# Kernel optimization log

Measured on AMD Instinct MI355X. Metric: run time of the kernel, lower is better.

The kernel has to match this reference:

```python
import jax, jax.numpy as jnp
import numpy as np

N_EXPERTS = 64
LN_EPS = 1e-5


def _layer_norm(x, gamma, beta, eps=LN_EPS):
    mu = jnp.mean(x, axis=-1, keepdims=True)
    var = jnp.mean(jnp.square(x - mu), axis=-1, keepdims=True)
    return (x - mu) * jax.lax.rsqrt(var + eps) * gamma + beta


def setup_inputs() -> dict:
    key = jax.random.key(0)
    ks = jax.random.split(key, 4)
    B, T, D, Ff = 2, 1024, 512, 2048
    x = jax.random.normal(ks[0], (B, T, D), dtype=jnp.float32)
    hex_weights = jax.random.uniform(ks[1], (B, T, N_EXPERTS), dtype=jnp.float32)
    W_in = jax.random.normal(ks[2], (N_EXPERTS, Ff, D), dtype=jnp.float32) * (D ** -0.5)
    b_in = jnp.zeros((N_EXPERTS, Ff), dtype=jnp.float32)
    W_out = jax.random.normal(ks[3], (N_EXPERTS, D, Ff), dtype=jnp.float32) * (Ff ** -0.5)
    b_out = jnp.zeros((N_EXPERTS, D), dtype=jnp.float32)
    ln_gamma = jnp.ones((D,), dtype=jnp.float32)
    ln_beta = jnp.zeros((D,), dtype=jnp.float32)
    return {"x": x, "hex_weights": hex_weights, "W_in": W_in, "b_in": b_in,
            "W_out": W_out, "b_out": b_out, "ln_gamma": ln_gamma,
            "ln_beta": ln_beta, "top_k": 4}


def reference(x, hex_weights, W_in, b_in, W_out, b_out, ln_gamma, ln_beta, top_k):
    B, T, D = x.shape
    N = B * T
    x_n = _layer_norm(x, ln_gamma, ln_beta)

    # top-k routing; renormalize the selected weights (matches torch topk + sum-norm)
    top_w, top_idx = jax.lax.top_k(hex_weights, top_k)          # (B,T,k)
    top_w = top_w / (jnp.sum(top_w, axis=-1, keepdims=True) + 1e-8)

    x_flat = x_n.reshape(N, D)
    # Scatter the k normalized weights into a dense (N, 64) routing matrix.
    # Non-selected experts get weight 0, so a dense per-expert sweep computes
    # EXACTLY the same combined output as the per-token gather in the original.
    w_full = jnp.zeros((N, N_EXPERTS), dtype=x.dtype)
    w_full = w_full.at[jnp.arange(N)[:, None], top_idx.reshape(N, top_k)].set(
        top_w.reshape(N, top_k))

    def body(acc, e):
        W_in_e, b_in_e, W_out_e, b_out_e, we = e  # we: (N,)
        h = jax.nn.silu(x_flat @ W_in_e.T + b_in_e)            # (N, d_ff)
        acc = acc + we[:, None] * (h @ W_out_e.T + b_out_e)    # (N, D)
        return acc, None

    acc, _ = jax.lax.scan(body, jnp.zeros_like(x_flat),
                          (W_in, b_in, W_out, b_out, w_full.T))
    return acc.reshape(B, T, D)
```

## Files before the change

kernel.cpp:

```cpp
#include <hip/hip_runtime.h>

#define NTOK 2048
#define DD   512
#define FFD  2048
#define NE   64
#define KSEL 4
#define NPAIR (NTOK*KSEL)
#define BM 192
#define BK 64
#define NT 128
#define HROWS (NPAIR + 256)

typedef short s16x8 __attribute__((ext_vector_type(8)));
typedef float f32x4 __attribute__((ext_vector_type(4)));

typedef const __attribute__((address_space(1))) char* gptr_t;
typedef __attribute__((address_space(3))) char* lptr_t;

static __device__ __forceinline__ unsigned short f2bf(float f) {
    unsigned int u = __builtin_bit_cast(unsigned int, f);
    u += 0x7FFFu + ((u >> 16) & 1u);
    return (unsigned short)(u >> 16);
}

static __device__ __forceinline__ void packwrite(char* base, int nn, int kb, float4 v) {
    unsigned int lo = (unsigned int)f2bf(v.x) | ((unsigned int)f2bf(v.y) << 16);
    unsigned int hi = (unsigned int)f2bf(v.z) | ((unsigned int)f2bf(v.w) << 16);
    *(uint2*)(base + nn * 128 + (kb ^ ((nn & 7) << 4))) = make_uint2(lo, hi);
}

__global__ __launch_bounds__(256) void k_ln_route(
    const float* __restrict__ x, const float* __restrict__ hw,
    const float* __restrict__ gamma, const float* __restrict__ beta,
    unsigned short* __restrict__ xn_bf, int* __restrict__ counts,
    int* __restrict__ tok_e, float* __restrict__ tok_w)
{
    const int t = blockIdx.x;
    const int tid = threadIdx.x;
    const float* xr = x + (size_t)t * DD;
    float v0 = xr[tid];
    float v1 = xr[tid + 256];
    float s = v0 + v1, s2 = v0*v0 + v1*v1;
    #pragma unroll
    for (int off = 32; off > 0; off >>= 1) {
        s  += __shfl_down(s, off);
        s2 += __shfl_down(s2, off);
    }
    __shared__ float rsum[4], rsum2[4];
    __shared__ float smu, srs;
    const int wid = tid >> 6, lane = tid & 63;
    if (lane == 0) { rsum[wid] = s; rsum2[wid] = s2; }
    __syncthreads();
    if (tid == 0) {
        float a = 0.f, b = 0.f;
        for (int i = 0; i < 4; ++i) { a += rsum[i]; b += rsum2[i]; }
        float mu  = a * (1.f / DD);
        float var = b * (1.f / DD) - mu * mu;
        smu = mu; srs = rsqrtf(var + 1e-5f);
    }
    __syncthreads();
    const float mu = smu, rstd = srs;
    xn_bf[(size_t)t*DD + tid]       = f2bf((v0 - mu) * rstd * gamma[tid]       + beta[tid]);
    xn_bf[(size_t)t*DD + tid + 256] = f2bf((v1 - mu) * rstd * gamma[tid + 256] + beta[tid + 256]);

    if (tid < 64) {
        float v = hw[(size_t)t*NE + tid];
        int   sel[KSEL]; float sw[KSEL];
        #pragma unroll
        for (int j = 0; j < KSEL; ++j) {
            float m = v; int mi = tid;
            #pragma unroll
            for (int off = 32; off > 0; off >>= 1) {
                float ov = __shfl_xor(m, off);
                int   oi = __shfl_xor(mi, off);
                if (ov > m || (ov == m && oi < mi)) { m = ov; mi = oi; }
            }
            if (tid == mi) v = -1e30f;
            sel[j] = mi; sw[j] = m;
        }
        if (tid == 0) {
            float ssum = sw[0] + sw[1] + sw[2] + sw[3];
            float inv = 1.f / (ssum + 1e-8f);
            #pragma unroll
            for (int j = 0; j < KSEL; ++j) {
                tok_e[t*KSEL + j] = sel[j];
                tok_w[t*KSEL + j] = sw[j] * inv;
                atomicAdd(&counts[sel[j]], 1);
            }
        }
    }
}

__global__ void k_scan(const int* __restrict__ counts, int* __restrict__ offs,
                       int* __restrict__ cursor, int* __restrict__ tile_e,
                       int* __restrict__ tile_r, int* __restrict__ ntiles)
{
    __shared__ int sc[NE], stc[NE];
    const int tid = threadIdx.x;
    sc[tid] = counts[tid];
    __syncthreads();
    int off = 0;
    for (int i = 0; i < tid; ++i) off += sc[i];
    offs[tid] = off; cursor[tid] = off;
    if (tid == NE-1) offs[NE] = off + sc[NE-1];
    int tc = (sc[tid] + BM - 1) / BM;
    stc[tid] = tc;
    __syncthreads();
    int toff = 0;
    for (int i = 0; i < tid; ++i) toff += stc[i];
    for (int j = 0; j < tc; ++j) { tile_e[toff + j] = tid; tile_r[toff + j] = off + j*BM; }
    if (tid == NE-1) *ntiles = toff + tc;
}

__global__ __launch_bounds__(256) void k_scatter(
    const int* __restrict__ tok_e, const float* __restrict__ tok_w,
    int* __restrict__ cursor, int* __restrict__ pair_tok,
    float* __restrict__ pair_w, int* __restrict__ inv)
{
    int i = blockIdx.x * 256 + threadIdx.x;
    if (i >= NPAIR) return;
    int t = i >> 2;
    int e = tok_e[i];
    int slot = atomicAdd(&cursor[e], 1);
    pair_tok[slot] = t;
    pair_w[slot] = tok_w[i];
    inv[i] = slot;
}

template<int KD, bool IS_IN, int NYG>
__global__ __launch_bounds__(256, 2) void k_moe_gemm(
    const unsigned short* __restrict__ Abf,
    const float* __restrict__ W, const float* __restrict__ bias,
    const int* __restrict__ tile_e, const int* __restrict__ tile_r,
    const int* __restrict__ ntiles, const int* __restrict__ offs,
    const int* __restrict__ pr_tok, const float* __restrict__ pr_w,
    unsigned short* __restrict__ Hout, float* __restrict__ Pout)
{
    constexpr int NK = KD / BK;
    const int ti = ((blockIdx.x >> 3) / NYG) * 8 + (blockIdx.x & 7);
    const int yg = (blockIdx.x >> 3) % NYG;
    if (ti >= *ntiles) return;
    const int e    = tile_e[ti];
    const int row0 = tile_r[ti];
    const int rend = offs[e + 1];
    const int n0   = yg * 64;
    const int NOUT = IS_IN ? FFD : DD;

    __shared__ __align__(16) unsigned short As[2 * BM * BK];
    __shared__ __align__(16) unsigned short Bs[2 * 64 * BK];

    const int tid  = threadIdx.x;
    const int lane = tid & 63, wave = tid >> 6;
    const int wmbase = wave * 48;

    const char* asrc[6];
    #pragma unroll
    for (int i = 0; i < 6; ++i) {
        int seg  = wave * 6 + i;
        int r    = seg * 8 + (lane >> 3);
        int grow = row0 + r;
        int cg   = (lane & 7) ^ (r & 7);
        size_t rowbase;
        if (IS_IN) {
            int tok = (grow < rend) ? pr_tok[grow] : pr_tok[row0];
            rowbase = (size_t)tok * (KD * 2);
        } else {
            rowbase = (size_t)grow * (KD * 2);
        }
        asrc[i] = (const char*)Abf + rowbase + (size_t)cg * 16;
    }

    const float* wsrc0 = W + (size_t)e * NOUT * KD + (size_t)(n0 + (tid >> 4)) * KD + (tid & 15) * 4;
    const int nb = tid >> 4;
    const int kb = (tid & 15) * 8;

    f32x4 acc[3][4];
    #pragma unroll
    for (int m = 0; m < 3; ++m)
        #pragma unroll
        for (int n = 0; n < 4; ++n)
            acc[m][n] = (f32x4){0.f, 0.f, 0.f, 0.f};

    float4 bset0[4], bset1[4];

    #pragma unroll
    for (int i = 0; i < 6; ++i)
        __builtin_amdgcn_global_load_lds((gptr_t)asrc[i],
            (lptr_t)((char*)As + (wave * 6 + i) * 1024), 16, 0, 0);
    __builtin_amdgcn_sched_barrier(0);
    #pragma unroll
    for (int i = 0; i < 4; ++i)
        bset0[i] = *(const float4*)(wsrc0 + (size_t)i * 16 * KD);
    __builtin_amdgcn_sched_barrier(0);
    #pragma unroll
    for (int i = 0; i < 4; ++i)
        bset1[i] = *(const float4*)(wsrc0 + (size_t)i * 16 * KD + BK);
    __builtin_amdgcn_sched_barrier(0);
    asm volatile("s_waitcnt vmcnt(4)" ::: "memory");
    __builtin_amdgcn_sched_barrier(0);
    #pragma unroll
    for (int i = 0; i < 4; ++i)
        packwrite((char*)Bs, nb + i * 16, kb, bset0[i]);

    int buf = 0;

#define GEMM_STEP(KT, SUSE, SISS)                                                        \
    {                                                                                    \
        if ((KT) == NK - 1) {                                                            \
            asm volatile("s_waitcnt vmcnt(0) lgkmcnt(0)" ::: "memory");                  \
        } else {                                                                         \
            asm volatile("s_waitcnt vmcnt(4) lgkmcnt(0)" ::: "memory");                  \
        }                                                                                \
        __builtin_amdgcn_s_barrier();                                                    \
        __builtin_amdgcn_sched_barrier(0);                                               \
        const int nbuf_ = buf ^ 1;                                                       \
        if ((KT) + 1 < NK) {                                                             \
            _Pragma("unroll")                                                            \
            for (int i = 0; i < 6; ++i)                                                  \
                __builtin_amdgcn_global_load_lds(                                        \
                    (gptr_t)(asrc[i] + (size_t)((KT) + 1) * BK * 2),                     \
                    (lptr_t)((char*)As + nbuf_ * (BM * BK * 2) + (wave * 6 + i) * 1024), \
                    16, 0, 0);                                                           \
        }                                                                                \
        __builtin_amdgcn_sched_barrier(0);                                               \
        if ((KT) + 2 < NK) {                                                             \
            _Pragma("unroll")                                                            \
            for (int i = 0; i < 4; ++i)                                                  \
                SISS[i] = *(const float4*)(wsrc0 + (size_t)i * 16 * KD + ((KT) + 2) * BK); \
        }                                                                                \
        __builtin_amdgcn_sched_barrier(0);                                               \
        {                                                                                \
            const char* Ab = (const char*)As + buf * (BM * BK * 2);                      \
            const char* Bb = (const char*)Bs + buf * (64 * BK * 2);                      \
            _Pragma("unroll")                                                            \
            for (int h = 0; h < 2; ++h) {                                                \
                s16x8 af[3], bfr[4];                                                     \
                const int koff = h * 64 + (lane >> 4) * 16;                              \
                _Pragma("unroll")                                                        \
                for (int m = 0; m < 3; ++m) {                                            \
                    int row = wmbase + m * 16 + (lane & 15);                             \
                    af[m] = *(const s16x8*)(Ab + row * 128 + (koff ^ ((row & 7) << 4))); \
                }                                                                        \
                _Pragma("unroll")                                                        \
                for (int n = 0; n < 4; ++n) {                                            \
                    int row = n * 16 + (lane & 15);                                      \
                    bfr[n] = *(const s16x8*)(Bb + row * 128 + (koff ^ ((row & 7) << 4)));\
                }                                                                        \
                _Pragma("unroll")                                                        \
                for (int m = 0; m < 3; ++m)                                              \
                    _Pragma("unroll")                                                    \
                    for (int n = 0; n < 4; ++n)                                          \
                        acc[m][n] = __builtin_amdgcn_mfma_f32_16x16x32_bf16(             \
                            af[m], bfr[n], acc[m][n], 0, 0, 0);                          \
            }                                                                            \
        }                                                                                \
        __builtin_amdgcn_sched_barrier(0);                                               \
        if ((KT) + 1 < NK) {                                                             \
            if ((KT) + 2 < NK) asm volatile("s_waitcnt vmcnt(10)" ::: "memory");         \
            else               asm volatile("s_waitcnt vmcnt(6)" ::: "memory");          \
            __builtin_amdgcn_sched_barrier(0);                                           \
            char* Bw = (char*)Bs + nbuf_ * (64 * BK * 2);                                \
            _Pragma("unroll")                                                            \
            for (int i = 0; i < 4; ++i)                                                  \
                packwrite(Bw, nb + i * 16, kb, SUSE[i]);                                 \
        }                                                                                \
        buf ^= 1;                                                                        \
    }

    for (int kt = 0; kt < NK; kt += 2) {
        GEMM_STEP(kt,     bset1, bset0);
        GEMM_STEP(kt + 1, bset0, bset1);
    }
#undef GEMM_STEP

    #pragma unroll
    for (int m = 0; m < 3; ++m) {
        #pragma unroll
        for (int r = 0; r < 4; ++r) {
            int row = row0 + wmbase + m * 16 + (lane >> 4) * 4 + r;
            if (row < rend) {
                if (IS_IN) {
                    #pragma unroll
                    for (int n = 0; n < 4; ++n) {
                        int f = n0 + n * 16 + (lane & 15);
                        float v = acc[m][n][r] + bias[e * FFD + f];
                        v = v / (1.f + __expf(-v));
                        Hout[(size_t)row * FFD + f] = f2bf(v);
                    }
                } else {
                    float pw = pr_w[row];
                    #pragma unroll
                    for (int n = 0; n < 4; ++n) {
                        int d = n0 + n * 16 + (lane & 15);
                        Pout[(size_t)row * DD + d] = (acc[m][n][r] + bias[e * DD + d]) * pw;
                    }
                }
            }
        }
    }
}

__global__ __launch_bounds__(128) void k_combine(
    const float* __restrict__ pout, const int* __restrict__ inv,
    float* __restrict__ out)
{
    const int t = blockIdx.x;
    const int tid = threadIdx.x;
    const float4* p0 = (const float4*)(pout + (size_t)inv[t*4+0]*DD);
    const float4* p1 = (const float4*)(pout + (size_t)inv[t*4+1]*DD);
    const float4* p2 = (const float4*)(pout + (size_t)inv[t*4+2]*DD);
    const float4* p3 = (const float4*)(pout + (size_t)inv[t*4+3]*DD);
    float4 a = p0[tid], b = p1[tid], c = p2[tid], d = p3[tid];
    float4 r;
    r.x = a.x + b.x + c.x + d.x;
    r.y = a.y + b.y + c.y + d.y;
    r.z = a.z + b.z + c.z + d.z;
    r.w = a.w + b.w + c.w + d.w;
    ((float4*)(out + (size_t)t*DD))[tid] = r;
}

extern "C" void kernel_launch(void* const* d_in, const int* in_sizes, int n_in,
                              void* d_out, int out_size, void* d_ws, size_t ws_size,
                              hipStream_t stream)
{
    const float* x     = (const float*)d_in[0];
    const float* hw    = (const float*)d_in[1];
    const float* Win   = (const float*)d_in[2];
    const float* bin   = (const float*)d_in[3];
    const float* Wout  = (const float*)d_in[4];
    const float* bout  = (const float*)d_in[5];
    const float* gamma = (const float*)d_in[6];
    const float* beta  = (const float*)d_in[7];
    float* out = (float*)d_out;

    char* ws = (char*)d_ws;
    size_t o = 0;
    unsigned short* xn_bf = (unsigned short*)(ws + o); o += (size_t)NTOK * DD * 2;
    unsigned short* H     = (unsigned short*)(ws + o); o += (size_t)HROWS * FFD * 2;
    float* pout   = (float*)(ws + o); o += (size_t)NPAIR * DD * 4;
    int*   counts = (int*)(ws + o);   o += 256;
    int*   offs   = (int*)(ws + o);   o += 512;
    int*   cursor = (int*)(ws + o);   o += 256;
    int*   tok_e  = (int*)(ws + o);   o += (size_t)NPAIR * 4;
    float* tok_w  = (float*)(ws + o); o += (size_t)NPAIR * 4;
    int*   inv    = (int*)(ws + o);   o += (size_t)NPAIR * 4;
    int*   pr_tok = (int*)(ws + o);   o += (size_t)NPAIR * 4;
    float* pr_w   = (float*)(ws + o); o += (size_t)NPAIR * 4;
    int*   tile_e = (int*)(ws + o);   o += 512;
    int*   tile_r = (int*)(ws + o);   o += 512;
    int*   ntiles = (int*)(ws + o);   o += 256;
    (void)ws_size; (void)in_sizes; (void)n_in; (void)out_size;

    hipMemsetAsync(counts, 0, 256, stream);
    k_ln_route<<<dim3(NTOK), dim3(256), 0, stream>>>(x, hw, gamma, beta, xn_bf, counts, tok_e, tok_w);
    k_scan<<<dim3(1), dim3(64), 0, stream>>>(counts, offs, cursor, tile_e, tile_r, ntiles);
    k_scatter<<<dim3(NPAIR/256), dim3(256), 0, stream>>>(tok_e, tok_w, cursor, pr_tok, pr_w, inv);

    k_moe_gemm<DD, true, FFD/64><<<dim3(NT * (FFD/64)), dim3(256), 0, stream>>>(
        xn_bf, Win, bin, tile_e, tile_r, ntiles, offs, pr_tok, pr_w, H, nullptr);
    k_moe_gemm<FFD, false, DD/64><<<dim3(NT * (DD/64)), dim3(256), 0, stream>>>(
        H, Wout, bout, tile_e, tile_r, ntiles, offs, pr_tok, pr_w, nullptr, pout);

    k_combine<<<dim3(NTOK), dim3(128), 0, stream>>>(pout, inv, out);
}
```

Before: 236.6 us.

## Double GEMM K-step to 128 and split MoE tiles across 8 waves

The MoE GEMM now processes a K-step of 128 per barrier, staged as two 64-wide halves in shared memory, and launches 512 threads (8 waves) per block instead of 256. The 192x64 output tile is split into a 4x2 grid of wave sub-tiles, so each wave holds a 3x2 accumulator instead of 3x4. This is meant to halve the number of barrier/sync iterations and add more waves for latency hiding. The costs are doubled LDS use per block (about 128KB for double buffering), which may cut blocks per CU, and fewer MFMAs per wave between barriers.

```diff
diff --git a/kernel.cpp b/kernel.cpp
--- a/kernel.cpp
+++ b/kernel.cpp
@@ -7,7 +7,7 @@
 #define KSEL 4
 #define NPAIR (NTOK*KSEL)
 #define BM 192
-#define BK 64
+#define BK 128
 #define NT 128
 #define HROWS (NPAIR + 256)
 
@@ -23,10 +23,10 @@
     return (unsigned short)(u >> 16);
 }
 
-static __device__ __forceinline__ void packwrite(char* base, int nn, int kb, float4 v) {
+static __device__ __forceinline__ void packwrite8(char* rowbase, int n, int kb, float4 v) {
     unsigned int lo = (unsigned int)f2bf(v.x) | ((unsigned int)f2bf(v.y) << 16);
     unsigned int hi = (unsigned int)f2bf(v.z) | ((unsigned int)f2bf(v.w) << 16);
-    *(uint2*)(base + nn * 128 + (kb ^ ((nn & 7) << 4))) = make_uint2(lo, hi);
+    *(uint2*)(rowbase + n * 128 + (kb ^ ((n & 7) << 4))) = make_uint2(lo, hi);
 }
 
 __global__ __launch_bounds__(256) void k_ln_route(
@@ -128,7 +128,7 @@
 }
 
 template<int KD, bool IS_IN, int NYG>
-__global__ __launch_bounds__(256, 2) void k_moe_gemm(
+__global__ __launch_bounds__(512, 2) void k_moe_gemm(
     const unsigned short* __restrict__ Abf,
     const float* __restrict__ W, const float* __restrict__ bias,
     const int* __restrict__ tile_e, const int* __restrict__ tile_r,
@@ -146,20 +146,22 @@
     const int n0   = yg * 64;
     const int NOUT = IS_IN ? FFD : DD;
 
-    __shared__ __align__(16) unsigned short As[2 * BM * BK];
-    __shared__ __align__(16) unsigned short Bs[2 * 64 * BK];
+    __shared__ __align__(16) unsigned short As[2 * 2 * BM * 64];
+    __shared__ __align__(16) unsigned short Bs[2 * 2 * 64 * 64];
 
     const int tid  = threadIdx.x;
     const int lane = tid & 63, wave = tid >> 6;
-    const int wmbase = wave * 48;
+    const int lr = lane & 15, lk = lane >> 4;
+    const int hsel = wave >> 2, wl = wave & 3;
+    const int rg = wave >> 1, cg = wave & 1;
 
     const char* asrc[6];
     #pragma unroll
     for (int i = 0; i < 6; ++i) {
-        int seg  = wave * 6 + i;
+        int seg  = wl * 6 + i;
         int r    = seg * 8 + (lane >> 3);
         int grow = row0 + r;
-        int cg   = (lane & 7) ^ (r & 7);
+        int cgk  = (lane & 7) ^ (r & 7);
         size_t rowbase;
         if (IS_IN) {
             int tok = (grow < rend) ? pr_tok[grow] : pr_tok[row0];
@@ -167,40 +169,44 @@
         } else {
             rowbase = (size_t)grow * (KD * 2);
         }
-        asrc[i] = (const char*)Abf + rowbase + (size_t)cg * 16;
-    }
-
-    const float* wsrc0 = W + (size_t)e * NOUT * KD + (size_t)(n0 + (tid >> 4)) * KD + (tid & 15) * 4;
-    const int nb = tid >> 4;
-    const int kb = (tid & 15) * 8;
-
-    f32x4 acc[3][4];
-    #pragma unroll
-    for (int m = 0; m < 3; ++m)
-        #pragma unroll
-        for (int n = 0; n < 4; ++n)
-            acc[m][n] = (f32x4){0.f, 0.f, 0.f, 0.f};
+        asrc[i] = (const char*)Abf + rowbase + (size_t)cgk * 16 + (size_t)hsel * 128;
+    }
+
+    const float* wsrc = W + (size_t)e * NOUT * KD + (size_t)(n0 + (tid >> 3)) * KD + (tid & 7) * 4;
+    const int bn = tid >> 3;
+    const int bj = (tid & 7) * 8;
+
+    f32x4 acc[3][2];
+    #pragma unroll
+    for (int m = 0; m < 3; ++m) {
+        acc[m][0] = (f32x4){0.f, 0.f, 0.f, 0.f};
+        acc[m][1] = (f32x4){0.f, 0.f, 0.f, 0.f};
+    }
 
     float4 bset0[4], bset1[4];
+
+#define BWRITE(BUFI, SET)                                                         \
+    _Pragma("unroll")                                                             \
+    for (int q = 0; q < 4; ++q)                                                   \
+        packwrite8((char*)Bs + (BUFI) * 16384 + (q >> 1) * 8192, bn,              \
+                   bj + (q & 1) * 64, SET[q]);
 
     #pragma unroll
     for (int i = 0; i < 6; ++i)
         __builtin_amdgcn_global_load_lds((gptr_t)asrc[i],
-            (lptr_t)((char*)As + (wave * 6 + i) * 1024), 16, 0, 0);
+            (lptr_t)((char*)As + hsel * 24576 + (wl * 6 + i) * 1024), 16, 0, 0);
     __builtin_amdgcn_sched_barrier(0);
     #pragma unroll
-    for (int i = 0; i < 4; ++i)
-        bset0[i] = *(const float4*)(wsrc0 + (size_t)i * 16 * KD);
+    for (int q = 0; q < 4; ++q)
+        bset0[q] = *(const float4*)(wsrc + q * 32);
     __builtin_amdgcn_sched_barrier(0);
     #pragma unroll
-    for (int i = 0; i < 4; ++i)
-        bset1[i] = *(const float4*)(wsrc0 + (size_t)i * 16 * KD + BK);
+    for (int q = 0; q < 4; ++q)
+        bset1[q] = *(const float4*)(wsrc + q * 32 + BK);
     __builtin_amdgcn_sched_barrier(0);
     asm volatile("s_waitcnt vmcnt(4)" ::: "memory");
     __builtin_amdgcn_sched_barrier(0);
-    #pragma unroll
-    for (int i = 0; i < 4; ++i)
-        packwrite((char*)Bs, nb + i * 16, kb, bset0[i]);
+    BWRITE(0, bset0);
 
     int buf = 0;
 
@@ -218,40 +224,41 @@
             _Pragma("unroll")                                                            \
             for (int i = 0; i < 6; ++i)                                                  \
                 __builtin_amdgcn_global_load_lds(                                        \
-                    (gptr_t)(asrc[i] + (size_t)((KT) + 1) * BK * 2),                     \
-                    (lptr_t)((char*)As + nbuf_ * (BM * BK * 2) + (wave * 6 + i) * 1024), \
-                    16, 0, 0);                                                           \
+                    (gptr_t)(asrc[i] + (size_t)((KT) + 1) * 256),                        \
+                    (lptr_t)((char*)As + nbuf_ * 49152 + hsel * 24576                    \
+                             + (wl * 6 + i) * 1024), 16, 0, 0);                          \
         }                                                                                \
         __builtin_amdgcn_sched_barrier(0);                                               \
         if ((KT) + 2 < NK) {                                                             \
             _Pragma("unroll")                                                            \
-            for (int i = 0; i < 4; ++i)                                                  \
-                SISS[i] = *(const float4*)(wsrc0 + (size_t)i * 16 * KD + ((KT) + 2) * BK); \
+            for (int q = 0; q < 4; ++q)                                                  \
+                SISS[q] = *(const float4*)(wsrc + q * 32 + ((KT) + 2) * BK);             \
         }                                                                                \
         __builtin_amdgcn_sched_barrier(0);                                               \
         {                                                                                \
-            const char* Ab = (const char*)As + buf * (BM * BK * 2);                      \
-            const char* Bb = (const char*)Bs + buf * (64 * BK * 2);                      \
             _Pragma("unroll")                                                            \
-            for (int h = 0; h < 2; ++h) {                                                \
-                s16x8 af[3], bfr[4];                                                     \
-                const int koff = h * 64 + (lane >> 4) * 16;                              \
+            for (int h2 = 0; h2 < 2; ++h2) {                                             \
+                const char* Ab = (const char*)As + buf * 49152 + h2 * 24576;             \
+                const char* Bb = (const char*)Bs + buf * 16384 + h2 * 8192;              \
                 _Pragma("unroll")                                                        \
-                for (int m = 0; m < 3; ++m) {                                            \
-                    int row = wmbase + m * 16 + (lane & 15);                             \
-                    af[m] = *(const s16x8*)(Ab + row * 128 + (koff ^ ((row & 7) << 4))); \
+                for (int h = 0; h < 2; ++h) {                                            \
+                    const int koff = h * 64 + lk * 16;                                   \
+                    const int swz  = koff ^ ((lr & 7) << 4);                             \
+                    s16x8 af[3], bfr[2];                                                 \
+                    _Pragma("unroll")                                                    \
+                    for (int m = 0; m < 3; ++m)                                          \
+                        af[m] = *(const s16x8*)(Ab + (rg * 48 + m * 16 + lr) * 128 + swz);\
+                    _Pragma("unroll")                                                    \
+                    for (int n = 0; n < 2; ++n)                                          \
+                        bfr[n] = *(const s16x8*)(Bb + (cg * 32 + n * 16 + lr) * 128 + swz);\
+                    _Pragma("unroll")                                                    \
+                    for (int m = 0; m < 3; ++m) {                                        \
+                        acc[m][0] = __builtin_amdgcn_mfma_f32_16x16x32_bf16(             \
+                            af[m], bfr[0], acc[m][0], 0, 0, 0);                          \
+                        acc[m][1] = __builtin_amdgcn_mfma_f32_16x16x32_bf16(             \
+                            af[m], bfr[1], acc[m][1], 0, 0, 0);                          \
+                    }                                                                    \
                 }                                                                        \
-                _Pragma("unroll")                                                        \
-                for (int n = 0; n < 4; ++n) {                                            \
-                    int row = n * 16 + (lane & 15);                                      \
-                    bfr[n] = *(const s16x8*)(Bb + row * 128 + (koff ^ ((row & 7) << 4)));\
-                }                                                                        \
-                _Pragma("unroll")                                                        \
-                for (int m = 0; m < 3; ++m)                                              \
-                    _Pragma("unroll")                                                    \
-                    for (int n = 0; n < 4; ++n)                                          \
-                        acc[m][n] = __builtin_amdgcn_mfma_f32_16x16x32_bf16(             \
-                            af[m], bfr[n], acc[m][n], 0, 0, 0);                          \
             }                                                                            \
         }                                                                                \
         __builtin_amdgcn_sched_barrier(0);                                               \
@@ -259,10 +266,7 @@
             if ((KT) + 2 < NK) asm volatile("s_waitcnt vmcnt(10)" ::: "memory");         \
             else               asm volatile("s_waitcnt vmcnt(6)" ::: "memory");          \
             __builtin_amdgcn_sched_barrier(0);                                           \
-            char* Bw = (char*)Bs + nbuf_ * (64 * BK * 2);                                \
-            _Pragma("unroll")                                                            \
-            for (int i = 0; i < 4; ++i)                                                  \
-                packwrite(Bw, nb + i * 16, kb, SUSE[i]);                                 \
+            BWRITE(nbuf_, SUSE);                                                         \
         }                                                                                \
         buf ^= 1;                                                                        \
     }
@@ -272,17 +276,18 @@
         GEMM_STEP(kt + 1, bset0, bset1);
     }
 #undef GEMM_STEP
+#undef BWRITE
 
     #pragma unroll
     for (int m = 0; m < 3; ++m) {
         #pragma unroll
         for (int r = 0; r < 4; ++r) {
-            int row = row0 + wmbase + m * 16 + (lane >> 4) * 4 + r;
+            int row = row0 + rg * 48 + m * 16 + lk * 4 + r;
             if (row < rend) {
                 if (IS_IN) {
                     #pragma unroll
-                    for (int n = 0; n < 4; ++n) {
-                        int f = n0 + n * 16 + (lane & 15);
+                    for (int n = 0; n < 2; ++n) {
+                        int f = n0 + cg * 32 + n * 16 + lr;
                         float v = acc[m][n][r] + bias[e * FFD + f];
                         v = v / (1.f + __expf(-v));
                         Hout[(size_t)row * FFD + f] = f2bf(v);
@@ -290,8 +295,8 @@
                 } else {
                     float pw = pr_w[row];
                     #pragma unroll
-                    for (int n = 0; n < 4; ++n) {
-                        int d = n0 + n * 16 + (lane & 15);
+                    for (int n = 0; n < 2; ++n) {
+                        int d = n0 + cg * 32 + n * 16 + lr;
                         Pout[(size_t)row * DD + d] = (acc[m][n][r] + bias[e * DD + d]) * pw;
                     }
                 }
@@ -356,9 +361,9 @@
     k_scan<<<dim3(1), dim3(64), 0, stream>>>(counts, offs, cursor, tile_e, tile_r, ntiles);
     k_scatter<<<dim3(NPAIR/256), dim3(256), 0, stream>>>(tok_e, tok_w, cursor, pr_tok, pr_w, inv);
 
-    k_moe_gemm<DD, true, FFD/64><<<dim3(NT * (FFD/64)), dim3(256), 0, stream>>>(
+    k_moe_gemm<DD, true, FFD/64><<<dim3(NT * (FFD/64)), dim3(512), 0, stream>>>(
         xn_bf, Win, bin, tile_e, tile_r, ntiles, offs, pr_tok, pr_w, H, nullptr);
-    k_moe_gemm<FFD, false, DD/64><<<dim3(NT * (DD/64)), dim3(256), 0, stream>>>(
+    k_moe_gemm<FFD, false, DD/64><<<dim3(NT * (DD/64)), dim3(512), 0, stream>>>(
         H, Wout, bout, tile_e, tile_r, ntiles, offs, pr_tok, pr_w, nullptr, pout);
 
     k_combine<<<dim3(NTOK), dim3(128), 0, stream>>>(pout, inv, out);
```

Result: slower. 256.6 us (+8.5%).
